# Performance work log

Hardware: AMD Instinct MI355X
Metric: run time of the kernel (lower is better)

## Reference

```python
import jax, jax.numpy as jnp
import numpy as np

B, S, D, H = 2, 2048, 1024, 16
DH = D // H


def setup_inputs() -> dict:
    key = jax.random.key(0)
    ks = jax.random.split(key, 12)
    sc = 1.0 / np.sqrt(D)
    inp = {
        "v": jax.random.normal(ks[0], (B, S, D), jnp.float32),
        "k": jax.random.normal(ks[1], (B, S, D), jnp.float32),
        "q": jax.random.normal(ks[2], (B, S, D), jnp.float32),
        # causal mask: 1 where attention is disallowed (j > i)
        "mask": jnp.triu(jnp.ones((S, S), jnp.float32), k=1)[None, None, :, :],
        "Wq": jax.random.normal(ks[3], (D, D), jnp.float32) * sc,
        "bq": jnp.zeros((D,), jnp.float32),
        "Wk": jax.random.normal(ks[4], (D, D), jnp.float32) * sc,
        "bk": jnp.zeros((D,), jnp.float32),
        "Wv": jax.random.normal(ks[5], (D, D), jnp.float32) * sc,
        "bv": jnp.zeros((D,), jnp.float32),
        "Wo": jax.random.normal(ks[6], (D, D), jnp.float32) * sc,
        "bo": jnp.zeros((D,), jnp.float32),
    }
    return inp


def _split_heads(x):
    # [B, S, D] -> [B, H, S, DH]
    b, s, _ = x.shape
    return x.reshape(b, s, H, DH).transpose(0, 2, 1, 3)


def reference(v, k, q, mask, Wq, bq, Wk, bk, Wv, bv, Wo, bo):
    Q = _split_heads(q @ Wq + bq)
    K = _split_heads(k @ Wk + bk)
    V = _split_heads(v @ Wv + bv)
    # scaled dot-product attention, logits [B, H, Sq, Sk]
    logits = jnp.einsum("bhqd,bhkd->bhqk", Q, K) / jnp.sqrt(jnp.float32(DH))
    logits = logits + mask * (-1e9)
    attn = jax.nn.softmax(logits, axis=-1)
    ctx = jnp.einsum("bhqk,bhkd->bhqd", attn, V)
    ctx = ctx.transpose(0, 2, 1, 3).reshape(ctx.shape[0], -1, D)  # [B, S, D]
    out = ctx @ Wo + bo
    return out, attn
```

## Files before the change

kernel.cpp:

```cpp
#include <hip/hip_runtime.h>
#include <stdint.h>


typedef __attribute__((ext_vector_type(8))) short short8;
typedef __attribute__((ext_vector_type(4))) float f32x4;

#define WS_QB   0u
#define WS_KB   8388608u
#define WS_VB   16777216u
#define WS_WQT  25165824u
#define WS_WKT  27262976u
#define WS_WVT  29360128u
#define WS_WOT  31457280u
#define WS_QH   33554432u
#define WS_KH   41943040u
#define WS_VT   50331648u
#define WS_CTX  58720256u

__device__ __forceinline__ short f2bf(float f){
  uint32_t u = __builtin_bit_cast(uint32_t, f);
  u += 0x7FFFu + ((u >> 16) & 1u);
  return (short)(u >> 16);
}

typedef __attribute__((address_space(1))) const uint32_t guint;
typedef __attribute__((address_space(3))) uint32_t luint;
__device__ __forceinline__ void load16(const void* g, void* l){
  __builtin_amdgcn_global_load_lds((guint*)g, (luint*)l, 16, 0, 0);
}

__global__ __launch_bounds__(256)
void cvt_bf16(const float* __restrict__ src, short* __restrict__ dst){
  int i = (blockIdx.x * 256 + threadIdx.x) * 8;
  f32x4 a = *(const f32x4*)(src + i);
  f32x4 b = *(const f32x4*)(src + i + 4);
  short8 o;
  o[0]=f2bf(a[0]); o[1]=f2bf(a[1]); o[2]=f2bf(a[2]); o[3]=f2bf(a[3]);
  o[4]=f2bf(b[0]); o[5]=f2bf(b[1]); o[6]=f2bf(b[2]); o[7]=f2bf(b[3]);
  *(short8*)(dst + i) = o;
}

__global__ __launch_bounds__(256)
void transpose_cvt(const float* __restrict__ W, short* __restrict__ Wt){
  __shared__ float tile[32][33];
  int tx = threadIdx.x, ty = threadIdx.y;
  int n0 = blockIdx.x * 32, k0 = blockIdx.y * 32;
  #pragma unroll
  for (int r2 = 0; r2 < 4; r2++)
    tile[ty*4+r2][tx] = W[(size_t)(k0 + ty*4 + r2) * 1024 + n0 + tx];
  __syncthreads();
  #pragma unroll
  for (int r2 = 0; r2 < 4; r2++)
    Wt[(size_t)(n0 + ty*4 + r2) * 1024 + k0 + tx] = f2bf(tile[tx][ty*4+r2]);
}

template<int MODE>
__global__ __launch_bounds__(256)
void gemm_bf16(const short* __restrict__ A, const short* __restrict__ Bt,
               const float* __restrict__ bias, void* __restrict__ outp)
{
  const int K = 1024;
  __shared__ short lds[2][2][4096];
  int bid = blockIdx.x;
  int swz = (bid & 7) * 32 + (bid >> 3);
  int bi = swz >> 3, bj = swz & 7;
  int r0 = bi * 128, c0 = bj * 128;
  int t = threadIdx.x;
  int w = t >> 6, l = t & 63;
  int kb4 = l >> 4, rr = l & 15;
  int wr = (w >> 1) * 64, wc = (w & 1) * 64;

  f32x4 acc[4][4];
  #pragma unroll
  for (int i = 0; i < 4; i++)
    #pragma unroll
    for (int j = 0; j < 4; j++) acc[i][j] = (f32x4){0.f,0.f,0.f,0.f};

  auto stage = [&](int buf, int k0){
    #pragma unroll
    for (int i = 0; i < 2; i++){
      int L = i * 4096 + t * 16;
      int kb = L >> 11;
      int row = (L >> 4) & 127;
      load16(A  + (size_t)(r0 + row) * K + k0 + kb * 8,
             (char*)(&lds[buf][0][0]) + i * 4096 + w * 1024);
      load16(Bt + (size_t)(c0 + row) * K + k0 + kb * 8,
             (char*)(&lds[buf][1][0]) + i * 4096 + w * 1024);
    }
  };

  stage(0, 0);
  __syncthreads();
  for (int kt = 0; kt < 32; kt++){
    if (kt + 1 < 32) stage((kt + 1) & 1, (kt + 1) * 32);
    const short* Al = &lds[kt & 1][0][0];
    const short* Bl = &lds[kt & 1][1][0];
    short8 af[4], bfr[4];
    #pragma unroll
    for (int i = 0; i < 4; i++)
      af[i] = *(const short8*)(Al + kb4 * 1024 + (wr + i*16 + rr) * 8);
    #pragma unroll
    for (int j = 0; j < 4; j++)
      bfr[j] = *(const short8*)(Bl + kb4 * 1024 + (wc + j*16 + rr) * 8);
    #pragma unroll
    for (int i = 0; i < 4; i++)
      #pragma unroll
      for (int j = 0; j < 4; j++)
        acc[i][j] = __builtin_amdgcn_mfma_f32_16x16x32_bf16(af[i], bfr[j], acc[i][j], 0, 0, 0);
    __syncthreads();
  }

  #pragma unroll
  for (int i = 0; i < 4; i++){
    #pragma unroll
    for (int j = 0; j < 4; j++){
      int colg = c0 + wc + j*16 + rr;
      float bv_ = bias[colg];
      #pragma unroll
      for (int r = 0; r < 4; r++){
        int rowg = r0 + wr + i*16 + kb4*4 + r;
        float val = acc[i][j][r] + bv_;
        if (MODE == 2){
          ((float*)outp)[(size_t)rowg * 1024 + colg] = val;
        } else {
          int bb = rowg >> 11, s = rowg & 2047, hh = colg >> 6, dh = colg & 63;
          if (MODE == 0)
            ((short*)outp)[((size_t)(bb*16 + hh) * 2048 + s) * 64 + dh] = f2bf(val);
          else
            ((short*)outp)[((size_t)(bb*16 + hh) * 64 + dh) * 2048 + s] = f2bf(val);
        }
      }
    }
  }
}

__global__ __launch_bounds__(256)
void attn_fused(const short* __restrict__ Qh, const short* __restrict__ Kh,
                const short* __restrict__ Vt, float* __restrict__ attn,
                short* __restrict__ ctx)
{
  __shared__ short Kl[2][4096];
  __shared__ short Vl[2][4096];
  __shared__ short Pl[4][1024];

  int qb = blockIdx.x, h = blockIdx.y, b = blockIdx.z;
  int bh = b * 16 + h;
  int t = threadIdx.x, w = t >> 6, l = t & 63;
  int kb4 = l >> 4, rr = l & 15;
  int q0 = qb * 64;
  int wq = q0 + w * 16;
  int nkt = qb + 1;

  const short* Qb = Qh + (size_t)bh * 2048 * 64;
  const short* Kb = Kh + (size_t)bh * 2048 * 64;
  const short* Vb = Vt + (size_t)bh * 64 * 2048;
  float* arow = attn + (size_t)bh * 2048 * 2048;

  short8 qf[2];
  #pragma unroll
  for (int ks = 0; ks < 2; ks++)
    qf[ks] = *(const short8*)(Qb + (size_t)(wq + rr) * 64 + ks * 32 + kb4 * 8);

  auto stageK = [&](int buf, int kt){
    #pragma unroll
    for (int i = 0; i < 2; i++){
      int L = i * 4096 + t * 16;
      int kb = L >> 10;
      int skl = (L >> 4) & 63;
      load16(Kb + (size_t)(kt * 64 + skl) * 64 + kb * 8,
             (char*)(&Kl[buf][0]) + i * 4096 + w * 1024);
    }
  };
  auto stageV = [&](int buf, int kt){
    #pragma unroll
    for (int i = 0; i < 2; i++){
      int L = i * 4096 + t * 16;
      int kb = L >> 10;
      int dh = (L >> 4) & 63;
      load16(Vb + (size_t)dh * 2048 + kt * 64 + kb * 8,
             (char*)(&Vl[buf][0]) + i * 4096 + w * 1024);
    }
  };

  float m[4], ls[4];
  #pragma unroll
  for (int r = 0; r < 4; r++){ m[r] = -__builtin_inff(); ls[r] = 0.f; }

  stageK(0, 0);
  __syncthreads();
  for (int kt = 0; kt < nkt; kt++){
    if (kt + 1 < nkt) stageK((kt + 1) & 1, kt + 1);
    const short* Kt = &Kl[kt & 1][0];
    float xs[4][4];
    #pragma unroll
    for (int fc = 0; fc < 4; fc++){
      f32x4 a = (f32x4){0.f,0.f,0.f,0.f};
      #pragma unroll
      for (int ks = 0; ks < 2; ks++){
        short8 kf = *(const short8*)(Kt + (ks*4 + kb4) * 512 + (fc*16 + rr) * 8);
        a = __builtin_amdgcn_mfma_f32_16x16x32_bf16(qf[ks], kf, a, 0, 0, 0);
      }
      int sk = kt * 64 + fc * 16 + rr;
      #pragma unroll
      for (int r = 0; r < 4; r++){
        int sq = wq + kb4 * 4 + r;
        float x = a[r] * 0.125f;
        xs[fc][r] = (sk > sq) ? -1e30f : x;
      }
    }
    #pragma unroll
    for (int r = 0; r < 4; r++){
      float tm = fmaxf(fmaxf(xs[0][r], xs[1][r]), fmaxf(xs[2][r], xs[3][r]));
      #pragma unroll
      for (int d = 1; d < 16; d <<= 1) tm = fmaxf(tm, __shfl_xor(tm, d, 64));
      float mn = fmaxf(m[r], tm);
      float corr = __expf(m[r] - mn);
      float s = __expf(xs[0][r]-mn) + __expf(xs[1][r]-mn)
              + __expf(xs[2][r]-mn) + __expf(xs[3][r]-mn);
      #pragma unroll
      for (int d = 1; d < 16; d <<= 1) s += __shfl_xor(s, d, 64);
      ls[r] = ls[r] * corr + s;
      m[r] = mn;
    }
    __syncthreads();
  }

  float rl[4];
  #pragma unroll
  for (int r = 0; r < 4; r++) rl[r] = 1.0f / ls[r];
  f32x4 cacc[4];
  #pragma unroll
  for (int j = 0; j < 4; j++) cacc[j] = (f32x4){0.f,0.f,0.f,0.f};

  stageK(0, 0); stageV(0, 0);
  __syncthreads();
  for (int kt = 0; kt < nkt; kt++){
    if (kt + 1 < nkt){ stageK((kt + 1) & 1, kt + 1); stageV((kt + 1) & 1, kt + 1); }
    const short* Kt  = &Kl[kt & 1][0];
    const short* Vtl = &Vl[kt & 1][0];
    #pragma unroll
    for (int fc = 0; fc < 4; fc++){
      f32x4 a = (f32x4){0.f,0.f,0.f,0.f};
      #pragma unroll
      for (int ks = 0; ks < 2; ks++){
        short8 kf = *(const short8*)(Kt + (ks*4 + kb4) * 512 + (fc*16 + rr) * 8);
        a = __builtin_amdgcn_mfma_f32_16x16x32_bf16(qf[ks], kf, a, 0, 0, 0);
      }
      int sk = kt * 64 + fc * 16 + rr;
      #pragma unroll
      for (int r = 0; r < 4; r++){
        int rowl = kb4 * 4 + r;
        int sq = wq + rowl;
        float x = a[r] * 0.125f;
        float p = (sk > sq) ? 0.f : __expf(x - m[r]) * rl[r];
        arow[(size_t)sq * 2048 + sk] = p;
        int csw = (fc * 16 + rr) ^ ((rowl & 7) << 3);
        Pl[w][rowl * 64 + csw] = f2bf(p);
      }
    }
    #pragma unroll
    for (int ks = 0; ks < 2; ks++){
      int kbl = ks * 4 + kb4;
      short8 pa = *(const short8*)(&Pl[w][rr * 64 + ((kbl ^ (rr & 7)) * 8)]);
      #pragma unroll
      for (int j = 0; j < 4; j++){
        short8 vf = *(const short8*)(Vtl + kbl * 512 + (j*16 + rr) * 8);
        cacc[j] = __builtin_amdgcn_mfma_f32_16x16x32_bf16(pa, vf, cacc[j], 0, 0, 0);
      }
    }
    __syncthreads();
  }

  for (int kt = nkt; kt < 32; kt++){
    #pragma unroll
    for (int r = 0; r < 4; r++){
      int sq = wq + kb4 * 4 + r;
      *(f32x4*)(arow + (size_t)sq * 2048 + kt * 64 + rr * 4) = (f32x4){0.f,0.f,0.f,0.f};
    }
  }

  #pragma unroll
  for (int j = 0; j < 4; j++){
    #pragma unroll
    for (int r = 0; r < 4; r++){
      int sq = wq + kb4 * 4 + r;
      int dg = h * 64 + j * 16 + rr;
      ctx[((size_t)b * 2048 + sq) * 1024 + dg] = f2bf(cacc[j][r]);
    }
  }
}

extern "C" void kernel_launch(void* const* d_in, const int* in_sizes, int n_in,
                              void* d_out, int out_size, void* d_ws, size_t ws_size,
                              hipStream_t stream)
{
  const float* v  = (const float*)d_in[0];
  const float* k  = (const float*)d_in[1];
  const float* q  = (const float*)d_in[2];
  const float* Wq = (const float*)d_in[4];
  const float* bq = (const float*)d_in[5];
  const float* Wk = (const float*)d_in[6];
  const float* bk = (const float*)d_in[7];
  const float* Wv = (const float*)d_in[8];
  const float* bv = (const float*)d_in[9];
  const float* Wo = (const float*)d_in[10];
  const float* bo = (const float*)d_in[11];

  char* ws = (char*)d_ws;
  short* qbuf = (short*)(ws + WS_QB);
  short* kbuf = (short*)(ws + WS_KB);
  short* vbuf = (short*)(ws + WS_VB);
  short* Wqt  = (short*)(ws + WS_WQT);
  short* Wkt  = (short*)(ws + WS_WKT);
  short* Wvt  = (short*)(ws + WS_WVT);
  short* Wot  = (short*)(ws + WS_WOT);
  short* Qh   = (short*)(ws + WS_QH);
  short* Kh   = (short*)(ws + WS_KH);
  short* Vt   = (short*)(ws + WS_VT);
  short* ctx  = (short*)(ws + WS_CTX);

  float* outp = (float*)d_out;
  float* attn = outp + 4194304;

  cvt_bf16<<<2048, 256, 0, stream>>>(q, qbuf);
  cvt_bf16<<<2048, 256, 0, stream>>>(k, kbuf);
  cvt_bf16<<<2048, 256, 0, stream>>>(v, vbuf);
  transpose_cvt<<<dim3(32,32), dim3(32,8), 0, stream>>>(Wq, Wqt);
  transpose_cvt<<<dim3(32,32), dim3(32,8), 0, stream>>>(Wk, Wkt);
  transpose_cvt<<<dim3(32,32), dim3(32,8), 0, stream>>>(Wv, Wvt);
  transpose_cvt<<<dim3(32,32), dim3(32,8), 0, stream>>>(Wo, Wot);

  gemm_bf16<0><<<256, 256, 0, stream>>>(qbuf, Wqt, bq, Qh);
  gemm_bf16<0><<<256, 256, 0, stream>>>(kbuf, Wkt, bk, Kh);
  gemm_bf16<1><<<256, 256, 0, stream>>>(vbuf, Wvt, bv, Vt);

  attn_fused<<<dim3(32,16,2), 256, 0, stream>>>(Qh, Kh, Vt, attn, ctx);

  gemm_bf16<2><<<256, 256, 0, stream>>>(ctx, Wot, bo, outp);
}
```

Baseline: 849.5 us.

## Merge QKV GEMMs, pair causal query blocks, and stage attention writes via LDS

Fuses the three projection GEMMs into one 768-block launch over concatenated transposed weights, and folds the 1/sqrt(dh) scale into Q. The attention kernel now processes two complementary query blocks per workgroup (qb and 31-qb) to balance causal work, masks only on the diagonal tile, and defers cross-lane softmax reductions to a single merge after the loop. Probability rows are written to global memory as coalesced float4 stores read back from the bf16 LDS tile, which changes attn output precision to bf16-rounded. The output GEMM uses 128x64 tiles for more blocks, and MFMA priority hints are added.

```diff
diff --git a/kernel.cpp b/kernel.cpp
--- a/kernel.cpp
+++ b/kernel.cpp
@@ -3,24 +3,27 @@
 
 
 typedef __attribute__((ext_vector_type(8))) short short8;
+typedef __attribute__((ext_vector_type(4))) short short4v;
 typedef __attribute__((ext_vector_type(4))) float f32x4;
 
-#define WS_QB   0u
-#define WS_KB   8388608u
-#define WS_VB   16777216u
-#define WS_WQT  25165824u
-#define WS_WKT  27262976u
-#define WS_WVT  29360128u
-#define WS_WOT  31457280u
-#define WS_QH   33554432u
-#define WS_KH   41943040u
-#define WS_VT   50331648u
-#define WS_CTX  58720256u
+#define WS_QB    0u
+#define WS_KB    8388608u
+#define WS_VB    16777216u
+#define WS_WQKVT 25165824u
+#define WS_WOT   31457280u
+#define WS_QH    33554432u
+#define WS_KH    41943040u
+#define WS_VT    50331648u
+#define WS_CTX   58720256u
 
 __device__ __forceinline__ short f2bf(float f){
   uint32_t u = __builtin_bit_cast(uint32_t, f);
   u += 0x7FFFu + ((u >> 16) & 1u);
   return (short)(u >> 16);
+}
+__device__ __forceinline__ float bf2f(short s){
+  uint32_t u = ((uint32_t)(uint16_t)s) << 16;
+  return __builtin_bit_cast(float, u);
 }
 
 typedef __attribute__((address_space(1))) const uint32_t guint;
@@ -54,17 +57,21 @@
     Wt[(size_t)(n0 + ty*4 + r2) * 1024 + k0 + tx] = f2bf(tile[tx][ty*4+r2]);
 }
 
-template<int MODE>
 __global__ __launch_bounds__(256)
-void gemm_bf16(const short* __restrict__ A, const short* __restrict__ Bt,
-               const float* __restrict__ bias, void* __restrict__ outp)
+void gemm_qkv(const short* __restrict__ qb_, const short* __restrict__ kb_,
+              const short* __restrict__ vb_, const short* __restrict__ Wt,
+              const float* __restrict__ bq, const float* __restrict__ bk,
+              const float* __restrict__ bv,
+              short* __restrict__ Qh, short* __restrict__ Kh, short* __restrict__ Vt)
 {
   const int K = 1024;
   __shared__ short lds[2][2][4096];
   int bid = blockIdx.x;
-  int swz = (bid & 7) * 32 + (bid >> 3);
-  int bi = swz >> 3, bj = swz & 7;
+  int swz = (bid & 7) * 96 + (bid >> 3);
+  int bi = swz / 24, bj = swz - bi * 24;
   int r0 = bi * 128, c0 = bj * 128;
+  int seg = bj >> 3;
+  const short* A = seg == 0 ? qb_ : seg == 1 ? kb_ : vb_;
   int t = threadIdx.x;
   int w = t >> 6, l = t & 63;
   int kb4 = l >> 4, rr = l & 15;
@@ -84,7 +91,7 @@
       int row = (L >> 4) & 127;
       load16(A  + (size_t)(r0 + row) * K + k0 + kb * 8,
              (char*)(&lds[buf][0][0]) + i * 4096 + w * 1024);
-      load16(Bt + (size_t)(c0 + row) * K + k0 + kb * 8,
+      load16(Wt + (size_t)(c0 + row) * K + k0 + kb * 8,
              (char*)(&lds[buf][1][0]) + i * 4096 + w * 1024);
     }
   };
@@ -110,25 +117,100 @@
     __syncthreads();
   }
 
+  const float* bias = seg == 0 ? bq : seg == 1 ? bk : bv;
+  float scale = seg == 0 ? 0.125f : 1.0f;
   #pragma unroll
   for (int i = 0; i < 4; i++){
     #pragma unroll
     for (int j = 0; j < 4; j++){
       int colg = c0 + wc + j*16 + rr;
-      float bv_ = bias[colg];
+      int cw = colg & 1023;
+      float bv_ = bias[cw];
       #pragma unroll
       for (int r = 0; r < 4; r++){
         int rowg = r0 + wr + i*16 + kb4*4 + r;
-        float val = acc[i][j][r] + bv_;
-        if (MODE == 2){
-          ((float*)outp)[(size_t)rowg * 1024 + colg] = val;
-        } else {
-          int bb = rowg >> 11, s = rowg & 2047, hh = colg >> 6, dh = colg & 63;
-          if (MODE == 0)
-            ((short*)outp)[((size_t)(bb*16 + hh) * 2048 + s) * 64 + dh] = f2bf(val);
-          else
-            ((short*)outp)[((size_t)(bb*16 + hh) * 64 + dh) * 2048 + s] = f2bf(val);
-        }
+        float val = (acc[i][j][r] + bv_) * scale;
+        int bb = rowg >> 11, s = rowg & 2047, hh = cw >> 6, dh = cw & 63;
+        if (seg == 0)
+          Qh[((size_t)(bb*16 + hh) * 2048 + s) * 64 + dh] = f2bf(val);
+        else if (seg == 1)
+          Kh[((size_t)(bb*16 + hh) * 2048 + s) * 64 + dh] = f2bf(val);
+        else
+          Vt[((size_t)(bb*16 + hh) * 64 + dh) * 2048 + s] = f2bf(val);
+      }
+    }
+  }
+}
+
+__global__ __launch_bounds__(256)
+void gemm_out(const short* __restrict__ A, const short* __restrict__ Bt,
+              const float* __restrict__ bias, float* __restrict__ outp)
+{
+  const int K = 1024;
+  __shared__ short ldsA[2][4096];
+  __shared__ short ldsB[2][2048];
+  int bid = blockIdx.x;
+  int swz = (bid & 7) * 64 + (bid >> 3);
+  int bi = swz >> 4, bj = swz & 15;
+  int r0 = bi * 128, c0 = bj * 64;
+  int t = threadIdx.x;
+  int w = t >> 6, l = t & 63;
+  int kb4 = l >> 4, rr = l & 15;
+  int wr = (w >> 1) * 64, wc = (w & 1) * 32;
+
+  f32x4 acc[4][2];
+  #pragma unroll
+  for (int i = 0; i < 4; i++)
+    #pragma unroll
+    for (int j = 0; j < 2; j++) acc[i][j] = (f32x4){0.f,0.f,0.f,0.f};
+
+  auto stage = [&](int buf, int k0){
+    #pragma unroll
+    for (int i = 0; i < 2; i++){
+      int L = i * 4096 + t * 16;
+      int kb = L >> 11;
+      int row = (L >> 4) & 127;
+      load16(A + (size_t)(r0 + row) * K + k0 + kb * 8,
+             (char*)(&ldsA[buf][0]) + i * 4096 + w * 1024);
+    }
+    int L = t * 16;
+    int kb = L >> 10;
+    int row = (L >> 4) & 63;
+    load16(Bt + (size_t)(c0 + row) * K + k0 + kb * 8,
+           (char*)(&ldsB[buf][0]) + w * 1024);
+  };
+
+  stage(0, 0);
+  __syncthreads();
+  for (int kt = 0; kt < 32; kt++){
+    if (kt + 1 < 32) stage((kt + 1) & 1, (kt + 1) * 32);
+    const short* Al = &ldsA[kt & 1][0];
+    const short* Bl = &ldsB[kt & 1][0];
+    short8 af[4], bfr[2];
+    #pragma unroll
+    for (int i = 0; i < 4; i++)
+      af[i] = *(const short8*)(Al + kb4 * 1024 + (wr + i*16 + rr) * 8);
+    #pragma unroll
+    for (int j = 0; j < 2; j++)
+      bfr[j] = *(const short8*)(Bl + kb4 * 512 + (wc + j*16 + rr) * 8);
+    #pragma unroll
+    for (int i = 0; i < 4; i++)
+      #pragma unroll
+      for (int j = 0; j < 2; j++)
+        acc[i][j] = __builtin_amdgcn_mfma_f32_16x16x32_bf16(af[i], bfr[j], acc[i][j], 0, 0, 0);
+    __syncthreads();
+  }
+
+  #pragma unroll
+  for (int i = 0; i < 4; i++){
+    #pragma unroll
+    for (int j = 0; j < 2; j++){
+      int colg = c0 + wc + j*16 + rr;
+      float bv_ = bias[colg];
+      #pragma unroll
+      for (int r = 0; r < 4; r++){
+        int rowg = r0 + wr + i*16 + kb4*4 + r;
+        outp[(size_t)rowg * 1024 + colg] = acc[i][j][r] + bv_;
       }
     }
   }
@@ -143,23 +225,15 @@
   __shared__ short Vl[2][4096];
   __shared__ short Pl[4][1024];
 
-  int qb = blockIdx.x, h = blockIdx.y, b = blockIdx.z;
+  int h = blockIdx.y, b = blockIdx.z;
   int bh = b * 16 + h;
   int t = threadIdx.x, w = t >> 6, l = t & 63;
   int kb4 = l >> 4, rr = l & 15;
-  int q0 = qb * 64;
-  int wq = q0 + w * 16;
-  int nkt = qb + 1;
 
   const short* Qb = Qh + (size_t)bh * 2048 * 64;
   const short* Kb = Kh + (size_t)bh * 2048 * 64;
   const short* Vb = Vt + (size_t)bh * 64 * 2048;
   float* arow = attn + (size_t)bh * 2048 * 2048;
-
-  short8 qf[2];
-  #pragma unroll
-  for (int ks = 0; ks < 2; ks++)
-    qf[ks] = *(const short8*)(Qb + (size_t)(wq + rr) * 64 + ks * 32 + kb4 * 8);
 
   auto stageK = [&](int buf, int kt){
     #pragma unroll
@@ -182,110 +256,143 @@
     }
   };
 
-  float m[4], ls[4];
-  #pragma unroll
-  for (int r = 0; r < 4; r++){ m[r] = -__builtin_inff(); ls[r] = 0.f; }
-
-  stageK(0, 0);
-  __syncthreads();
-  for (int kt = 0; kt < nkt; kt++){
-    if (kt + 1 < nkt) stageK((kt + 1) & 1, kt + 1);
-    const short* Kt = &Kl[kt & 1][0];
-    float xs[4][4];
-    #pragma unroll
-    for (int fc = 0; fc < 4; fc++){
-      f32x4 a = (f32x4){0.f,0.f,0.f,0.f};
+  for (int sel = 0; sel < 2; sel++){
+    int qb = sel ? 31 - blockIdx.x : blockIdx.x;
+    int q0 = qb * 64;
+    int wq = q0 + w * 16;
+    int nkt = qb + 1;
+
+    short8 qf[2];
+    #pragma unroll
+    for (int ks = 0; ks < 2; ks++)
+      qf[ks] = *(const short8*)(Qb + (size_t)(wq + rr) * 64 + ks * 32 + kb4 * 8);
+
+    float m[4], ls[4];
+    #pragma unroll
+    for (int r = 0; r < 4; r++){ m[r] = -1e30f; ls[r] = 0.f; }
+
+    stageK(0, 0);
+    __syncthreads();
+    for (int kt = 0; kt < nkt; kt++){
+      if (kt + 1 < nkt) stageK((kt + 1) & 1, kt + 1);
+      const short* Kt = &Kl[kt & 1][0];
+      bool diag = (kt == qb);
+      float xs[4][4];
+      #pragma unroll
+      for (int fc = 0; fc < 4; fc++){
+        f32x4 a = (f32x4){0.f,0.f,0.f,0.f};
+        #pragma unroll
+        for (int ks = 0; ks < 2; ks++){
+          short8 kf = *(const short8*)(Kt + (ks*4 + kb4) * 512 + (fc*16 + rr) * 8);
+          a = __builtin_amdgcn_mfma_f32_16x16x32_bf16(qf[ks], kf, a, 0, 0, 0);
+        }
+        #pragma unroll
+        for (int r = 0; r < 4; r++){
+          float x = a[r];
+          if (diag) x = (fc*16 + rr > w*16 + kb4*4 + r) ? -1e30f : x;
+          xs[fc][r] = x;
+        }
+      }
+      #pragma unroll
+      for (int r = 0; r < 4; r++){
+        float tm = fmaxf(fmaxf(xs[0][r], xs[1][r]), fmaxf(xs[2][r], xs[3][r]));
+        float mn = fmaxf(m[r], tm);
+        float corr = __expf(m[r] - mn);
+        float s = __expf(xs[0][r]-mn) + __expf(xs[1][r]-mn)
+                + __expf(xs[2][r]-mn) + __expf(xs[3][r]-mn);
+        ls[r] = ls[r] * corr + s;
+        m[r] = mn;
+      }
+      __syncthreads();
+    }
+    #pragma unroll
+    for (int r = 0; r < 4; r++){
+      #pragma unroll
+      for (int d = 1; d < 16; d <<= 1){
+        float mo = __shfl_xor(m[r], d, 64);
+        float lo = __shfl_xor(ls[r], d, 64);
+        float mn = fmaxf(m[r], mo);
+        ls[r] = ls[r] * __expf(m[r] - mn) + lo * __expf(mo - mn);
+        m[r] = mn;
+      }
+    }
+    float rl[4];
+    #pragma unroll
+    for (int r = 0; r < 4; r++) rl[r] = 1.0f / ls[r];
+
+    f32x4 cacc[4];
+    #pragma unroll
+    for (int j = 0; j < 4; j++) cacc[j] = (f32x4){0.f,0.f,0.f,0.f};
+
+    stageK(0, 0); stageV(0, 0);
+    __syncthreads();
+    for (int kt = 0; kt < nkt; kt++){
+      if (kt + 1 < nkt){ stageK((kt + 1) & 1, kt + 1); stageV((kt + 1) & 1, kt + 1); }
+      const short* Kt  = &Kl[kt & 1][0];
+      const short* Vtl = &Vl[kt & 1][0];
+      bool diag = (kt == qb);
+      #pragma unroll
+      for (int fc = 0; fc < 4; fc++){
+        f32x4 a = (f32x4){0.f,0.f,0.f,0.f};
+        #pragma unroll
+        for (int ks = 0; ks < 2; ks++){
+          short8 kf = *(const short8*)(Kt + (ks*4 + kb4) * 512 + (fc*16 + rr) * 8);
+          a = __builtin_amdgcn_mfma_f32_16x16x32_bf16(qf[ks], kf, a, 0, 0, 0);
+        }
+        #pragma unroll
+        for (int r = 0; r < 4; r++){
+          int rowl = kb4 * 4 + r;
+          float p = __expf(a[r] - m[r]) * rl[r];
+          if (diag) p = (fc*16 + rr > w*16 + rowl) ? 0.f : p;
+          Pl[w][rowl * 64 + ((fc*16 + rr) ^ ((rowl & 7) << 3))] = f2bf(p);
+        }
+      }
+      __builtin_amdgcn_s_setprio(1);
       #pragma unroll
       for (int ks = 0; ks < 2; ks++){
-        short8 kf = *(const short8*)(Kt + (ks*4 + kb4) * 512 + (fc*16 + rr) * 8);
-        a = __builtin_amdgcn_mfma_f32_16x16x32_bf16(qf[ks], kf, a, 0, 0, 0);
-      }
-      int sk = kt * 64 + fc * 16 + rr;
+        int kbl = ks * 4 + kb4;
+        short8 pa = *(const short8*)(&Pl[w][rr * 64 + ((kbl * 8) ^ ((rr & 7) << 3))]);
+        #pragma unroll
+        for (int j = 0; j < 4; j++){
+          short8 vf = *(const short8*)(Vtl + kbl * 512 + (j*16 + rr) * 8);
+          cacc[j] = __builtin_amdgcn_mfma_f32_16x16x32_bf16(pa, vf, cacc[j], 0, 0, 0);
+        }
+      }
+      __builtin_amdgcn_s_setprio(0);
+      {
+        int srow = l >> 2;
+        int c4 = (l & 3) * 4;
+        float* base = arow + (size_t)(wq + srow) * 2048 + kt * 64;
+        int s_ = (srow & 7) << 3;
+        #pragma unroll
+        for (int part = 0; part < 4; part++){
+          int cb = part * 16 + c4;
+          short4v pv = *(const short4v*)(&Pl[w][srow * 64 + (cb ^ s_)]);
+          f32x4 o;
+          o[0] = bf2f(pv[0]); o[1] = bf2f(pv[1]);
+          o[2] = bf2f(pv[2]); o[3] = bf2f(pv[3]);
+          *(f32x4*)(base + cb) = o;
+        }
+      }
+      __syncthreads();
+    }
+
+    for (int kt = nkt; kt < 32; kt++){
       #pragma unroll
       for (int r = 0; r < 4; r++){
         int sq = wq + kb4 * 4 + r;
-        float x = a[r] * 0.125f;
-        xs[fc][r] = (sk > sq) ? -1e30f : x;
-      }
-    }
-    #pragma unroll
-    for (int r = 0; r < 4; r++){
-      float tm = fmaxf(fmaxf(xs[0][r], xs[1][r]), fmaxf(xs[2][r], xs[3][r]));
-      #pragma unroll
-      for (int d = 1; d < 16; d <<= 1) tm = fmaxf(tm, __shfl_xor(tm, d, 64));
-      float mn = fmaxf(m[r], tm);
-      float corr = __expf(m[r] - mn);
-      float s = __expf(xs[0][r]-mn) + __expf(xs[1][r]-mn)
-              + __expf(xs[2][r]-mn) + __expf(xs[3][r]-mn);
-      #pragma unroll
-      for (int d = 1; d < 16; d <<= 1) s += __shfl_xor(s, d, 64);
-      ls[r] = ls[r] * corr + s;
-      m[r] = mn;
-    }
-    __syncthreads();
-  }
-
-  float rl[4];
-  #pragma unroll
-  for (int r = 0; r < 4; r++) rl[r] = 1.0f / ls[r];
-  f32x4 cacc[4];
-  #pragma unroll
-  for (int j = 0; j < 4; j++) cacc[j] = (f32x4){0.f,0.f,0.f,0.f};
-
-  stageK(0, 0); stageV(0, 0);
-  __syncthreads();
-  for (int kt = 0; kt < nkt; kt++){
-    if (kt + 1 < nkt){ stageK((kt + 1) & 1, kt + 1); stageV((kt + 1) & 1, kt + 1); }
-    const short* Kt  = &Kl[kt & 1][0];
-    const short* Vtl = &Vl[kt & 1][0];
-    #pragma unroll
-    for (int fc = 0; fc < 4; fc++){
-      f32x4 a = (f32x4){0.f,0.f,0.f,0.f};
-      #pragma unroll
-      for (int ks = 0; ks < 2; ks++){
-        short8 kf = *(const short8*)(Kt + (ks*4 + kb4) * 512 + (fc*16 + rr) * 8);
-        a = __builtin_amdgcn_mfma_f32_16x16x32_bf16(qf[ks], kf, a, 0, 0, 0);
-      }
-      int sk = kt * 64 + fc * 16 + rr;
+        *(f32x4*)(arow + (size_t)sq * 2048 + kt * 64 + rr * 4) = (f32x4){0.f,0.f,0.f,0.f};
+      }
+    }
+
+    #pragma unroll
+    for (int j = 0; j < 4; j++){
       #pragma unroll
       for (int r = 0; r < 4; r++){
-        int rowl = kb4 * 4 + r;
-        int sq = wq + rowl;
-        float x = a[r] * 0.125f;
-        float p = (sk > sq) ? 0.f : __expf(x - m[r]) * rl[r];
-        arow[(size_t)sq * 2048 + sk] = p;
-        int csw = (fc * 16 + rr) ^ ((rowl & 7) << 3);
-        Pl[w][rowl * 64 + csw] = f2bf(p);
-      }
-    }
-    #pragma unroll
-    for (int ks = 0; ks < 2; ks++){
-      int kbl = ks * 4 + kb4;
-      short8 pa = *(const short8*)(&Pl[w][rr * 64 + ((kbl ^ (rr & 7)) * 8)]);
-      #pragma unroll
-      for (int j = 0; j < 4; j++){
-        short8 vf = *(const short8*)(Vtl + kbl * 512 + (j*16 + rr) * 8);
-        cacc[j] = __builtin_amdgcn_mfma_f32_16x16x32_bf16(pa, vf, cacc[j], 0, 0, 0);
-      }
-    }
-    __syncthreads();
-  }
-
-  for (int kt = nkt; kt < 32; kt++){
-    #pragma unroll
-    for (int r = 0; r < 4; r++){
-      int sq = wq + kb4 * 4 + r;
-      *(f32x4*)(arow + (size_t)sq * 2048 + kt * 64 + rr * 4) = (f32x4){0.f,0.f,0.f,0.f};
-    }
-  }
-
-  #pragma unroll
-  for (int j = 0; j < 4; j++){
-    #pragma unroll
-    for (int r = 0; r < 4; r++){
-      int sq = wq + kb4 * 4 + r;
-      int dg = h * 64 + j * 16 + rr;
-      ctx[((size_t)b * 2048 + sq) * 1024 + dg] = f2bf(cacc[j][r]);
+        int sq = wq + kb4 * 4 + r;
+        int dg = h * 64 + j * 16 + rr;
+        ctx[((size_t)b * 2048 + sq) * 1024 + dg] = f2bf(cacc[j][r]);
+      }
     }
   }
 }
@@ -307,17 +414,15 @@
   const float* bo = (const float*)d_in[11];
 
   char* ws = (char*)d_ws;
-  short* qbuf = (short*)(ws + WS_QB);
-  short* kbuf = (short*)(ws + WS_KB);
-  short* vbuf = (short*)(ws + WS_VB);
-  short* Wqt  = (short*)(ws + WS_WQT);
-  short* Wkt  = (short*)(ws + WS_WKT);
-  short* Wvt  = (short*)(ws + WS_WVT);
-  short* Wot  = (short*)(ws + WS_WOT);
-  short* Qh   = (short*)(ws + WS_QH);
-  short* Kh   = (short*)(ws + WS_KH);
-  short* Vt   = (short*)(ws + WS_VT);
-  short* ctx  = (short*)(ws + WS_CTX);
+  short* qbuf  = (short*)(ws + WS_QB);
+  short* kbuf  = (short*)(ws + WS_KB);
+  short* vbuf  = (short*)(ws + WS_VB);
+  short* Wqkvt = (short*)(ws + WS_WQKVT);
+  short* Wot   = (short*)(ws + WS_WOT);
+  short* Qh    = (short*)(ws + WS_QH);
+  short* Kh    = (short*)(ws + WS_KH);
+  short* Vt    = (short*)(ws + WS_VT);
+  short* ctx   = (short*)(ws + WS_CTX);
 
   float* outp = (float*)d_out;
   float* attn = outp + 4194304;
@@ -325,16 +430,14 @@
   cvt_bf16<<<2048, 256, 0, stream>>>(q, qbuf);
   cvt_bf16<<<2048, 256, 0, stream>>>(k, kbuf);
   cvt_bf16<<<2048, 256, 0, stream>>>(v, vbuf);
-  transpose_cvt<<<dim3(32,32), dim3(32,8), 0, stream>>>(Wq, Wqt);
-  transpose_cvt<<<dim3(32,32), dim3(32,8), 0, stream>>>(Wk, Wkt);
-  transpose_cvt<<<dim3(32,32), dim3(32,8), 0, stream>>>(Wv, Wvt);
+  transpose_cvt<<<dim3(32,32), dim3(32,8), 0, stream>>>(Wq, Wqkvt);
+  transpose_cvt<<<dim3(32,32), dim3(32,8), 0, stream>>>(Wk, Wqkvt + 1048576);
+  transpose_cvt<<<dim3(32,32), dim3(32,8), 0, stream>>>(Wv, Wqkvt + 2097152);
   transpose_cvt<<<dim3(32,32), dim3(32,8), 0, stream>>>(Wo, Wot);
 
-  gemm_bf16<0><<<256, 256, 0, stream>>>(qbuf, Wqt, bq, Qh);
-  gemm_bf16<0><<<256, 256, 0, stream>>>(kbuf, Wkt, bk, Kh);
-  gemm_bf16<1><<<256, 256, 0, stream>>>(vbuf, Wvt, bv, Vt);
-
-  attn_fused<<<dim3(32,16,2), 256, 0, stream>>>(Qh, Kh, Vt, attn, ctx);
-
-  gemm_bf16<2><<<256, 256, 0, stream>>>(ctx, Wot, bo, outp);
-}
+  gemm_qkv<<<768, 256, 0, stream>>>(qbuf, kbuf, vbuf, Wqkvt, bq, bk, bv, Qh, Kh, Vt);
+
+  attn_fused<<<dim3(16,16,2), 256, 0, stream>>>(Qh, Kh, Vt, attn, ctx);
+
+  gemm_out<<<512, 256, 0, stream>>>(ctx, Wot, bo, outp);
+}
```

Measured after the change: 808.5 us. 4.8% less time.
